# Kernel optimization log

Measured on AMD Instinct MI355X. Metric: run time of the kernel, lower is better.

## Reference

```python
import jax, jax.numpy as jnp
import numpy as np

C = 512
NH = 8
GROUPS = 32
EPS = 1e-5


def setup_inputs() -> dict:
    key = jax.random.key(0)
    ks = jax.random.split(key, 7)
    B, T, H, W = 4, 24, 32, 32
    x = jax.random.normal(ks[0], (B, C, T, H, W), dtype=jnp.float32)
    gn_w = jnp.ones((C,), jnp.float32)
    gn_b = jnp.zeros((C,), jnp.float32)
    # 1x1 Conv1d weights stored as [out_ch, in_ch] (kernel dim of size 1 dropped)
    qkv_w = jax.random.normal(ks[1], (3 * C, C), dtype=jnp.float32) / np.sqrt(C)
    qkv_b = jax.random.normal(ks[2], (3 * C,), dtype=jnp.float32) * 0.02
    proj_w = jax.random.normal(ks[3], (C, C), dtype=jnp.float32) / np.sqrt(C)
    proj_b = jax.random.normal(ks[4], (C,), dtype=jnp.float32) * 0.02
    return {"x": x, "gn_w": gn_w, "gn_b": gn_b, "qkv_w": qkv_w,
            "qkv_b": qkv_b, "proj_w": proj_w, "proj_b": proj_b}


def reference(x, gn_w, gn_b, qkv_w, qkv_b, proj_w, proj_b):
    B, Cc, T, H, W = x.shape
    hd = Cc // NH
    # [B,C,T,H,W] -> [B*H*W, C, T]
    xf = jnp.transpose(x, (0, 3, 4, 1, 2)).reshape(B * H * W, Cc, T)
    # GroupNorm over (C/G, T) per group
    xg = xf.reshape(-1, GROUPS, Cc // GROUPS, T)
    mean = xg.mean(axis=(2, 3), keepdims=True)
    var = xg.var(axis=(2, 3), keepdims=True)
    xn = ((xg - mean) * jax.lax.rsqrt(var + EPS)).reshape(-1, Cc, T)
    xn = xn * gn_w[:, None] + gn_b[:, None]
    # 1x1 conv QKV: [n, 3C, T]
    qkv = jnp.einsum('nct,dc->ndt', xn, qkv_w) + qkv_b[:, None]
    qkv = qkv.reshape(-1, 3, NH, hd, T)
    q, k, v = qkv[:, 0], qkv[:, 1], qkv[:, 2]  # each [n, h, d, T]
    scale = 1.0 / np.sqrt(hd)
    attn = jax.nn.softmax(jnp.einsum('nhdt,nhds->nhts', q, k) * scale, axis=-1)
    out = jnp.einsum('nhts,nhds->nhtd', attn, v)        # [n, h, T, d]
    out = out.transpose(0, 2, 1, 3).reshape(-1, T, Cc)   # [n, T, C]
    out = out.transpose(0, 2, 1)                         # [n, C, T]
    out = jnp.einsum('nct,dc->ndt', out, proj_w) + proj_b[:, None]
    out = out.reshape(B, H, W, Cc, T).transpose(0, 3, 4, 1, 2)
    return x + out
```

## Files before the change

### kernel.cpp

```cpp
#include <hip/hip_runtime.h>
#include <hip/hip_bf16.h>
#include <stdint.h>

#define C_    512
#define T_    24
#define HWSZ  1024
#define NN    4096
#define JTOT  98304
#define EPSV  1e-5f

typedef short short8 __attribute__((ext_vector_type(8)));
typedef short short4v __attribute__((ext_vector_type(4)));
typedef float f32x4 __attribute__((ext_vector_type(4)));
typedef float f32x2 __attribute__((ext_vector_type(2)));
typedef __bf16 bf16x2 __attribute__((ext_vector_type(2)));

typedef __attribute__((address_space(1))) const uint32_t glob_u32;
typedef __attribute__((address_space(3))) uint32_t lds_u32;

#if __has_builtin(__builtin_amdgcn_fdot2_f32_bf16)
#define HAS_DOT2 1
#else
#define HAS_DOT2 0
#endif

__device__ __forceinline__ unsigned short f2bf(float f) {
  union { float f; unsigned u; } v; v.f = f;
  unsigned r = v.u + 0x7fffu + ((v.u >> 16) & 1u);
  return (unsigned short)(r >> 16);
}
__device__ __forceinline__ float bf2f(unsigned short b) {
  union { unsigned u; float f; } v; v.u = ((unsigned)b) << 16;
  return v.f;
}
__device__ __forceinline__ float bflo(uint32_t u) {
  union { unsigned u; float f; } v; v.u = u << 16; return v.f;
}
__device__ __forceinline__ float bfhi(uint32_t u) {
  union { unsigned u; float f; } v; v.u = u & 0xffff0000u; return v.f;
}
__device__ __forceinline__ uint32_t pkbf(float a, float b) {
  return (uint32_t)f2bf(a) | ((uint32_t)f2bf(b) << 16);
}
__device__ __forceinline__ bf16x2 asbf2(uint32_t u) {
  union { uint32_t u; bf16x2 v; } c; c.u = u; return c.v;
}

__device__ __forceinline__ void gload_lds16(const void* g, void* l) {
  __builtin_amdgcn_global_load_lds((glob_u32*)g, (lds_u32*)l, 16, 0, 0);
}

__global__ void k_cvt(const float* __restrict__ qkvw, const float* __restrict__ projw,
                      unsigned short* __restrict__ qkvw_bf, unsigned short* __restrict__ projw_bf) {
  int i = blockIdx.x * 256 + threadIdx.x;
  if (i < 786432) qkvw_bf[i] = f2bf(qkvw[i]);
  if (i < 262144) projw_bf[i] = f2bf(projw[i]);
}

__global__ __launch_bounds__(256) void k_stats(const float* __restrict__ x,
                                               float* __restrict__ mean, float* __restrict__ rstd) {
  int bid = blockIdx.x;
  int g = bid & 31, hwt = (bid >> 5) & 15, b = bid >> 9;
  int tid = threadIdx.x, lane = tid & 63, grp = tid >> 6;
  int hw = hwt * 64 + lane;
  float s = 0.f, sq = 0.f;
  for (int ct = grp; ct < 384; ct += 4) {
    int c = g * 16 + ct / 24;
    int t = ct % 24;
    float v = x[((size_t)((b * 512 + c) * 24 + t) << 10) + hw];
    s += v; sq += v * v;
  }
  __shared__ float ls[4][64], lq[4][64];
  ls[grp][lane] = s; lq[grp][lane] = sq;
  __syncthreads();
  if (tid < 64) {
    float S = ls[0][tid] + ls[1][tid] + ls[2][tid] + ls[3][tid];
    float Q = lq[0][tid] + lq[1][tid] + lq[2][tid] + lq[3][tid];
    float m = S * (1.f / 384.f);
    float var = Q * (1.f / 384.f) - m * m;
    int n = b * HWSZ + hwt * 64 + tid;
    mean[n * 32 + g] = m;
    rstd[n * 32 + g] = rsqrtf(var + EPSV);
  }
}

__global__ __launch_bounds__(256) void k_norm(const float* __restrict__ x,
                                              const float* __restrict__ mean, const float* __restrict__ rstd,
                                              const float* __restrict__ gnw, const float* __restrict__ gnb,
                                              unsigned short* __restrict__ xn) {
  __shared__ unsigned short xs[64][260];
  const int bid = blockIdx.x;
  const int hwt = bid & 15;
  const int chalf = (bid >> 4) & 1;
  const int tb = bid >> 5;
  const int t = tb % 24, b = tb / 24;
  const int hw0 = hwt * 64;
  const int tid = threadIdx.x;
  const int w = tid >> 6, lane = tid & 63;

  const int cslot = w * 4 + (lane >> 4);
  const int hwr = (lane & 15) * 4;
#pragma unroll
  for (int k = 0; k < 8; ++k) {
    const int crel = k * 32 + cslot * 2;
    const int c = chalf * 256 + crel;
    const float4 v0 = *reinterpret_cast<const float4*>(
        &x[(((size_t)(b * 512 + c) * 24 + t) << 10) + hw0 + hwr]);
    const float4 v1 = *reinterpret_cast<const float4*>(
        &x[(((size_t)(b * 512 + c + 1) * 24 + t) << 10) + hw0 + hwr]);
    *reinterpret_cast<uint32_t*>(&xs[hwr + 0][crel]) = pkbf(v0.x, v1.x);
    *reinterpret_cast<uint32_t*>(&xs[hwr + 1][crel]) = pkbf(v0.y, v1.y);
    *reinterpret_cast<uint32_t*>(&xs[hwr + 2][crel]) = pkbf(v0.z, v1.z);
    *reinterpret_cast<uint32_t*>(&xs[hwr + 3][crel]) = pkbf(v0.w, v1.w);
  }

  const int crel8 = (lane & 31) * 8;
  const int c8 = chalf * 256 + crel8;
  const int g = c8 >> 4;
  float gw[8], gb[8];
#pragma unroll
  for (int i = 0; i < 8; ++i) { gw[i] = gnw[c8 + i]; gb[i] = gnb[c8 + i]; }
  float mm[8], rr[8];
#pragma unroll
  for (int p = 0; p < 8; ++p) {
    const int nrel = (p * 4 + w) * 2 + (lane >> 5);
    const int ng = b * HWSZ + hw0 + nrel;
    mm[p] = mean[ng * 32 + g];
    rr[p] = rstd[ng * 32 + g];
  }
  __syncthreads();

#pragma unroll
  for (int p = 0; p < 8; ++p) {
    const int nrel = (p * 4 + w) * 2 + (lane >> 5);
    const short4v lo = *reinterpret_cast<const short4v*>(&xs[nrel][crel8]);
    const short4v hi = *reinterpret_cast<const short4v*>(&xs[nrel][crel8 + 4]);
    float y[8];
#pragma unroll
    for (int i = 0; i < 4; ++i) {
      y[i]     = (bf2f((unsigned short)lo[i]) - mm[p]) * rr[p] * gw[i]     + gb[i];
      y[i + 4] = (bf2f((unsigned short)hi[i]) - mm[p]) * rr[p] * gw[i + 4] + gb[i + 4];
    }
    uint4 wv;
    wv.x = pkbf(y[0], y[1]);
    wv.y = pkbf(y[2], y[3]);
    wv.z = pkbf(y[4], y[5]);
    wv.w = pkbf(y[6], y[7]);
    const size_t j = (size_t)t * NN + b * HWSZ + hw0 + nrel;
    *reinterpret_cast<uint4*>(&xn[j * C_ + c8]) = wv;
  }
}

#define STAGE8(mat, half, tile, Gptr, row0)                                           \
  {                                                                                   \
    unsigned short* _l = &lds[(((tile) & 1) * 2 + (mat))][half][(w * 2) * 512];       \
    const unsigned short* _g = (Gptr) +                                               \
        (size_t)((row0) + (half) * 128 + (w * 2) * 8 + srow) * 512 +                  \
        (tile) * 64 + sslot * 8;                                                      \
    gload_lds16(_g, _l);                                                              \
    gload_lds16(_g + 8 * 512, _l + 512);                                              \
  }

__global__ __launch_bounds__(512, 2) void k_gemm8(
    const unsigned short* __restrict__ A,
    const unsigned short* __restrict__ B,
    const float* __restrict__ bias,
    uint32_t* __restrict__ outP) {
  __shared__ __attribute__((aligned(16))) unsigned short lds[4][2][8192];
  const int bid = blockIdx.x;
  const int cpx = 2304 >> 3;
  const int lid = (bid & 7) * cpx + (bid >> 3);
  const int mt = lid % 6, jt = lid / 6;
  const int m0 = mt * 256, j0 = jt * 256;
  const int tid = threadIdx.x;
  const int w = tid >> 6, lane = tid & 63;
  const int l16 = lane & 15, lqq = lane >> 4;
  const int wm = w >> 2, wn = w & 3;
  const int srow = lane >> 3;
  const int sslot = (lane & 7) ^ srow;
  const int k0off = l16 * 64 + ((lqq ^ (l16 & 7)) * 8);
  const int k1off = l16 * 64 + (((lqq + 4) ^ (l16 & 7)) * 8);

  f32x4 acc[8][4];
#pragma unroll
  for (int i = 0; i < 8; ++i)
#pragma unroll
    for (int j = 0; j < 4; ++j) acc[i][j] = {0.f, 0.f, 0.f, 0.f};

  STAGE8(0, 0, 0, A, m0); STAGE8(0, 1, 0, A, m0);
  STAGE8(1, 0, 0, B, j0); STAGE8(1, 1, 0, B, j0);
  STAGE8(0, 0, 1, A, m0); STAGE8(0, 1, 1, A, m0);
  STAGE8(1, 0, 1, B, j0);
  asm volatile("s_waitcnt vmcnt(6)" ::: "memory");
  __builtin_amdgcn_s_barrier();

  for (int t = 0; t < 8; ++t) {
    const int buf = t & 1;
    const unsigned short* Ab = &lds[buf * 2 + 0][wm][0];
    const unsigned short* Bb = &lds[buf * 2 + 1][wn >> 1][(wn & 1) * 4096];
    short8 a[8][2], bb[4][2];
#pragma unroll
    for (int rr = 0; rr < 8; ++rr) {
      a[rr][0] = *reinterpret_cast<const short8*>(Ab + rr * 1024 + k0off);
      a[rr][1] = *reinterpret_cast<const short8*>(Ab + rr * 1024 + k1off);
    }
#pragma unroll
    for (int cc = 0; cc < 2; ++cc) {
      bb[cc][0] = *reinterpret_cast<const short8*>(Bb + cc * 1024 + k0off);
      bb[cc][1] = *reinterpret_cast<const short8*>(Bb + cc * 1024 + k1off);
    }
    if (t < 7) STAGE8(1, 1, t + 1, B, j0);
    asm volatile("" ::: "memory");
    __builtin_amdgcn_s_barrier();
    asm volatile("s_waitcnt lgkmcnt(0)" ::: "memory");
    __builtin_amdgcn_sched_barrier(0);
    __builtin_amdgcn_s_setprio(1);
#pragma unroll
    for (int rr = 0; rr < 4; ++rr)
#pragma unroll
      for (int cc = 0; cc < 2; ++cc) {
        acc[rr][cc] = __builtin_amdgcn_mfma_f32_16x16x32_bf16(a[rr][0], bb[cc][0], acc[rr][cc], 0, 0, 0);
        acc[rr][cc] = __builtin_amdgcn_mfma_f32_16x16x32_bf16(a[rr][1], bb[cc][1], acc[rr][cc], 0, 0, 0);
      }
    __builtin_amdgcn_s_setprio(0);
    asm volatile("" ::: "memory");
    __builtin_amdgcn_s_barrier();
#pragma unroll
    for (int cc = 2; cc < 4; ++cc) {
      bb[cc][0] = *reinterpret_cast<const short8*>(Bb + cc * 1024 + k0off);
      bb[cc][1] = *reinterpret_cast<const short8*>(Bb + cc * 1024 + k1off);
    }
    if (t < 6) STAGE8(0, 0, t + 2, A, m0);
    asm volatile("" ::: "memory");
    __builtin_amdgcn_s_barrier();
    asm volatile("s_waitcnt lgkmcnt(0)" ::: "memory");
    __builtin_amdgcn_sched_barrier(0);
    __builtin_amdgcn_s_setprio(1);
#pragma unroll
    for (int rr = 0; rr < 4; ++rr)
#pragma unroll
      for (int cc = 2; cc < 4; ++cc) {
        acc[rr][cc] = __builtin_amdgcn_mfma_f32_16x16x32_bf16(a[rr][0], bb[cc][0], acc[rr][cc], 0, 0, 0);
        acc[rr][cc] = __builtin_amdgcn_mfma_f32_16x16x32_bf16(a[rr][1], bb[cc][1], acc[rr][cc], 0, 0, 0);
      }
    __builtin_amdgcn_s_setprio(0);
    asm volatile("" ::: "memory");
    __builtin_amdgcn_s_barrier();
    if (t < 6) STAGE8(0, 1, t + 2, A, m0);
    asm volatile("" ::: "memory");
    __builtin_amdgcn_s_barrier();
    __builtin_amdgcn_s_setprio(1);
#pragma unroll
    for (int rr = 4; rr < 8; ++rr)
#pragma unroll
      for (int cc = 0; cc < 2; ++cc) {
        acc[rr][cc] = __builtin_amdgcn_mfma_f32_16x16x32_bf16(a[rr][0], bb[cc][0], acc[rr][cc], 0, 0, 0);
        acc[rr][cc] = __builtin_amdgcn_mfma_f32_16x16x32_bf16(a[rr][1], bb[cc][1], acc[rr][cc], 0, 0, 0);
      }
    __builtin_amdgcn_s_setprio(0);
    asm volatile("" ::: "memory");
    __builtin_amdgcn_s_barrier();
    if (t < 6) STAGE8(1, 0, t + 2, B, j0);
    asm volatile("" ::: "memory");
    __builtin_amdgcn_s_barrier();
    __builtin_amdgcn_s_setprio(1);
#pragma unroll
    for (int rr = 4; rr < 8; ++rr)
#pragma unroll
      for (int cc = 2; cc < 4; ++cc) {
        acc[rr][cc] = __builtin_amdgcn_mfma_f32_16x16x32_bf16(a[rr][0], bb[cc][0], acc[rr][cc], 0, 0, 0);
        acc[rr][cc] = __builtin_amdgcn_mfma_f32_16x16x32_bf16(a[rr][1], bb[cc][1], acc[rr][cc], 0, 0, 0);
      }
    __builtin_amdgcn_s_setprio(0);
    asm volatile("" ::: "memory");
    if (t < 6) {
      asm volatile("s_waitcnt vmcnt(6)" ::: "memory");
    } else if (t == 6) {
      asm volatile("s_waitcnt vmcnt(0)" ::: "memory");
    }
    __builtin_amdgcn_s_barrier();
  }

#pragma unroll
  for (int rr = 0; rr < 8; ++rr) {
#pragma unroll
    for (int cc = 0; cc < 4; ++cc) {
      const int row = m0 + wm * 128 + rr * 16 + lqq * 4;
      const int col = j0 + wn * 64 + cc * 16 + l16;
      const int t_ = col >> 12, n = col & 4095;
      const int mat = row >> 9;
      const int hh = (row >> 6) & 7;
      const int d = row & 63;
      const int ch = d >> 3;
      const int dp = (d & 7) >> 1;
      const size_t blk = (size_t)((((mat * 8 + hh) * 8 + ch) * 4 + dp) * 24 + t_);
      const float v0 = acc[rr][cc][0] + bias[row];
      const float v1 = acc[rr][cc][1] + bias[row + 1];
      const float v2 = acc[rr][cc][2] + bias[row + 2];
      const float v3 = acc[rr][cc][3] + bias[row + 3];
      outP[blk * 4096 + n] = pkbf(v0, v1);
      outP[(blk + 24) * 4096 + n] = pkbf(v2, v3);
    }
  }
}

__global__ __launch_bounds__(256, 3) void k_proj(
    const unsigned short* __restrict__ A,
    const unsigned short* __restrict__ B,
    const float* __restrict__ bias,
    const float* __restrict__ xres,
    float* __restrict__ outf) {
  __shared__ __attribute__((aligned(16))) unsigned short As[2][8192];
  const int bid = blockIdx.x;
  const int cpx = 3072 >> 3;
  const int lid = (bid & 7) * cpx + (bid >> 3);
  const int mt = lid & 3, jt = lid >> 2;
  const int m0 = mt * 128, j0 = jt * 128;
  const int tid = threadIdx.x;
  const int w = tid >> 6, lane = tid & 63;
  const int l16 = lane & 15, lqq = lane >> 4;
  const int wm = w >> 1, wn = w & 1;
  const int srow8 = lane >> 3;
  const int sslot = (lane & 7) ^ srow8;
  const int k0off = l16 * 64 + ((lqq ^ (l16 & 7)) * 8);
  const int k1off = l16 * 64 + (((lqq + 4) ^ (l16 & 7)) * 8);

  f32x4 acc[4][4];
#pragma unroll
  for (int i = 0; i < 4; ++i)
#pragma unroll
    for (int j = 0; j < 4; ++j) acc[i][j] = {0.f, 0.f, 0.f, 0.f};

#define PSTAGE(buf, tile)                                                             \
  {                                                                                   \
    _Pragma("unroll")                                                                 \
    for (int m_ = 0; m_ < 4; ++m_) {                                                  \
      unsigned short* _l = &As[buf][m_ * 2048 + w * 512];                             \
      const unsigned short* _g = A +                                                  \
          (size_t)(m0 + m_ * 32 + w * 8 + srow8) * 512 + (tile) * 64 + sslot * 8;     \
      gload_lds16(_g, _l);                                                            \
    }                                                                                 \
  }

#define LOADB(dst, tt)                                                                \
  {                                                                                   \
    _Pragma("unroll")                                                                 \
    for (int cc = 0; cc < 4; ++cc) {                                                  \
      const int jj_ = j0 + wn * 64 + cc * 16 + l16;                                   \
      _Pragma("unroll")                                                               \
      for (int ks = 0; ks < 2; ++ks)                                                  \
        dst[cc][ks] = *reinterpret_cast<const short8*>(                               \
            &B[((size_t)((tt) * 8 + ks * 4 + lqq) * JTOT + jj_) * 8]);                \
    }                                                                                 \
  }

#define PSTEP(t, CUR, NXT)                                                            \
  {                                                                                   \
    if ((t) < 7) { PSTAGE(((t) + 1) & 1, (t) + 1); LOADB(NXT, (t) + 1); }             \
    const unsigned short* Ab = &As[(t) & 1][(wm * 64) * 64];                          \
    _Pragma("unroll")                                                                 \
    for (int rr = 0; rr < 4; ++rr) {                                                  \
      short8 a0 = *reinterpret_cast<const short8*>(Ab + rr * 1024 + k0off);           \
      short8 a1 = *reinterpret_cast<const short8*>(Ab + rr * 1024 + k1off);           \
      _Pragma("unroll")                                                               \
      for (int cc = 0; cc < 4; ++cc) {                                                \
        acc[rr][cc] = __builtin_amdgcn_mfma_f32_16x16x32_bf16(a0, CUR[cc][0], acc[rr][cc], 0, 0, 0); \
        acc[rr][cc] = __builtin_amdgcn_mfma_f32_16x16x32_bf16(a1, CUR[cc][1], acc[rr][cc], 0, 0, 0); \
      }                                                                               \
    }                                                                                 \
    __syncthreads();                                                                  \
  }

  short8 bbA[4][2], bbB[4][2];
  PSTAGE(0, 0);
  LOADB(bbA, 0);
  __syncthreads();

  PSTEP(0, bbA, bbB);
  PSTEP(1, bbB, bbA);
  PSTEP(2, bbA, bbB);
  PSTEP(3, bbB, bbA);
  PSTEP(4, bbA, bbB);
  PSTEP(5, bbB, bbA);
  PSTEP(6, bbA, bbB);
  PSTEP(7, bbB, bbA);

#pragma unroll
  for (int mi = 0; mi < 4; ++mi) {
#pragma unroll
    for (int ni = 0; ni < 4; ++ni) {
      const int dbase = m0 + wm * 64 + mi * 16 + lqq * 4;
      const int jj = j0 + wn * 64 + ni * 16 + l16;
      const int t_ = jj >> 12, n = jj & 4095;
      const int b_ = n >> 10, hw = n & 1023;
#pragma unroll
      for (int r = 0; r < 4; ++r) {
        size_t o = (((size_t)(b_ * 512 + dbase + r) * 24 + t_) << 10) + hw;
        outf[o] = xres[o] + acc[mi][ni][r] + bias[dbase + r];
      }
    }
  }
}

__global__ __launch_bounds__(512) void k_attn(const uint32_t* __restrict__ qkvP,
                                              unsigned short* __restrict__ aoC) {
  __shared__ uint32_t kq[2][4][24][64];
  const int ntile = blockIdx.x, h = blockIdx.y;
  const int n0 = ntile * 64;
  const int tid = threadIdx.x;
  const int lane = tid & 63, slot = tid >> 6;
  const int t0 = slot * 3;
  uint32_t* kqf = &kq[0][0][0][0];
  const int BLK = 4 * 24 * 4096;
  const size_t bQ = (size_t)((0 * 8 + h) * 8) * BLK;
  const size_t bK = (size_t)((1 * 8 + h) * 8) * BLK;
  const size_t bV = (size_t)((2 * 8 + h) * 8) * BLK;
  const int ub = tid & 448;

#define STAGE_QK(c_)                                                                  \
  {                                                                                   \
    const size_t cbk = bK + (size_t)(c_) * BLK;                                       \
    const size_t cbq = bQ + (size_t)(c_) * BLK;                                       \
    _Pragma("unroll")                                                                 \
    for (int p = 0; p < 3; ++p) {                                                     \
      const int u = p * 512 + tid;                                                    \
      gload_lds16(qkvP + cbk + (u >> 4) * 4096 + n0 + (u & 15) * 4,                   \
                  kqf + (size_t)(p * 512 + ub) * 4);                                  \
    }                                                                                 \
    _Pragma("unroll")                                                                 \
    for (int p = 0; p < 3; ++p) {                                                     \
      const int u = p * 512 + tid;                                                    \
      gload_lds16(qkvP + cbq + (u >> 4) * 4096 + n0 + (u & 15) * 4,                   \
                  kqf + (size_t)(1536 + p * 512 + ub) * 4);                           \
    }                                                                                 \
  }

#define STAGE_V(c_)                                                                   \
  {                                                                                   \
    const size_t cbv = bV + (size_t)(c_) * BLK;                                       \
    _Pragma("unroll")                                                                 \
    for (int p = 0; p < 3; ++p) {                                                     \
      const int u = p * 512 + tid;                                                    \
      gload_lds16(qkvP + cbv + (u >> 4) * 4096 + n0 + (u & 15) * 4,                   \
                  kqf + (size_t)(p * 512 + ub) * 4);                                  \
    }                                                                                 \
  }

  float S[3][24];
#pragma unroll
  for (int a = 0; a < 3; ++a)
#pragma unroll
    for (int s = 0; s < 24; ++s) S[a][s] = 0.f;

  STAGE_QK(0);
  __syncthreads();
  for (int c = 0; c < 8; ++c) {
    uint32_t qw[3][4];
#pragma unroll
    for (int dp = 0; dp < 4; ++dp)
#pragma unroll
      for (int a = 0; a < 3; ++a)
        qw[a][dp] = kq[1][dp][t0 + a][lane];
#if !HAS_DOT2
    float qf[3][8];
#pragma unroll
    for (int dp = 0; dp < 4; ++dp)
#pragma unroll
      for (int a = 0; a < 3; ++a) {
        qf[a][2 * dp]     = bflo(qw[a][dp]);
        qf[a][2 * dp + 1] = bfhi(qw[a][dp]);
      }
#endif
#pragma unroll
    for (int dp = 0; dp < 4; ++dp) {
#pragma unroll
      for (int s = 0; s < 24; ++s) {
        const uint32_t kpr = kq[0][dp][s][lane];
#if HAS_DOT2
        const bf16x2 k2 = asbf2(kpr);
        S[0][s] = __builtin_amdgcn_fdot2_f32_bf16(asbf2(qw[0][dp]), k2, S[0][s], false);
        S[1][s] = __builtin_amdgcn_fdot2_f32_bf16(asbf2(qw[1][dp]), k2, S[1][s], false);
        S[2][s] = __builtin_amdgcn_fdot2_f32_bf16(asbf2(qw[2][dp]), k2, S[2][s], false);
#else
        const float k0 = bflo(kpr), k1 = bfhi(kpr);
        S[0][s] = fmaf(qf[0][2 * dp], k0, S[0][s]);
        S[0][s] = fmaf(qf[0][2 * dp + 1], k1, S[0][s]);
        S[1][s] = fmaf(qf[1][2 * dp], k0, S[1][s]);
        S[1][s] = fmaf(qf[1][2 * dp + 1], k1, S[1][s]);
        S[2][s] = fmaf(qf[2][2 * dp], k0, S[2][s]);
        S[2][s] = fmaf(qf[2][2 * dp + 1], k1, S[2][s]);
#endif
      }
    }
    __syncthreads();
    if (c < 7) {
      STAGE_QK(c + 1);
      __syncthreads();
    }
  }

#pragma unroll
  for (int a = 0; a < 3; ++a) {
    float mx = S[a][0];
#pragma unroll
    for (int s = 1; s < 24; ++s) mx = fmaxf(mx, S[a][s]);
    float sum = 0.f;
#pragma unroll
    for (int s = 0; s < 24; ++s) {
      float e = __expf((S[a][s] - mx) * 0.125f);
      S[a][s] = e; sum += e;
    }
    float inv = 1.f / sum;
#pragma unroll
    for (int s = 0; s < 24; ++s) S[a][s] *= inv;
  }

  STAGE_V(0);
  __syncthreads();
  for (int c = 0; c < 8; ++c) {
    f32x2 o2[3][4];
#pragma unroll
    for (int a = 0; a < 3; ++a)
#pragma unroll
      for (int dp = 0; dp < 4; ++dp) o2[a][dp] = {0.f, 0.f};
#pragma unroll
    for (int dp = 0; dp < 4; ++dp) {
#pragma unroll
      for (int s = 0; s < 24; ++s) {
        const uint32_t vpr = kq[0][dp][s][lane];
        f32x2 v2;
        v2.x = bflo(vpr);
        v2.y = bfhi(vpr);
        o2[0][dp] += S[0][s] * v2;
        o2[1][dp] += S[1][s] * v2;
        o2[2][dp] += S[2][s] * v2;
      }
    }
#pragma unroll
    for (int a = 0; a < 3; ++a) {
      uint4 wv;
      wv.x = pkbf(o2[a][0].x, o2[a][0].y);
      wv.y = pkbf(o2[a][1].x, o2[a][1].y);
      wv.z = pkbf(o2[a][2].x, o2[a][2].y);
      wv.w = pkbf(o2[a][3].x, o2[a][3].y);
      const size_t unit = (size_t)(h * 8 + c) * JTOT + (size_t)(t0 + a) * NN + n0 + lane;
      *reinterpret_cast<uint4*>(&aoC[unit * 8]) = wv;
    }
    __syncthreads();
    if (c < 7) {
      STAGE_V(c + 1);
      __syncthreads();
    }
  }
}

extern "C" void kernel_launch(void* const* d_in, const int* in_sizes, int n_in,
                              void* d_out, int out_size, void* d_ws, size_t ws_size,
                              hipStream_t stream) {
  (void)in_sizes; (void)n_in; (void)out_size; (void)ws_size;
  const float* x     = (const float*)d_in[0];
  const float* gnw   = (const float*)d_in[1];
  const float* gnb   = (const float*)d_in[2];
  const float* qkvw  = (const float*)d_in[3];
  const float* qkvb  = (const float*)d_in[4];
  const float* projw = (const float*)d_in[5];
  const float* projb = (const float*)d_in[6];
  float* out = (float*)d_out;
  char* ws = (char*)d_ws;

  unsigned short* qkvw_bf = (unsigned short*)(ws);
  unsigned short* projw_bf = (unsigned short*)(ws + 1572864);
  float* mean = (float*)(ws + 2097152);
  float* rstd = (float*)(ws + 2621440);
  unsigned short* xn  = (unsigned short*)(ws + 3145728);
  uint32_t* qkvP = (uint32_t*)(ws + 3145728 + 100663296);

  k_cvt<<<dim3(3072), dim3(256), 0, stream>>>(qkvw, projw, qkvw_bf, projw_bf);
  k_stats<<<dim3(2048), dim3(256), 0, stream>>>(x, mean, rstd);
  k_norm<<<dim3(3072), dim3(256), 0, stream>>>(x, mean, rstd, gnw, gnb, xn);
  k_gemm8<<<dim3(2304), dim3(512), 0, stream>>>(qkvw_bf, xn, qkvb, qkvP);
  k_attn<<<dim3(64, 8), dim3(512), 0, stream>>>(qkvP, xn);
  k_proj<<<dim3(3072), dim3(256), 0, stream>>>(projw_bf, xn, projb, x, out);
}
```

Before: 533.0 us.

## Interleave QKV packed layout so each token's 8 head dims form one 16-byte unit

Changes the QKV GEMM epilogue to write the four bf16 pairs of an 8-dim chunk contiguously per (t, n), using 8-byte vector stores in place of two scattered 4-byte stores. The attention kernel now loads these 16-byte units with global-to-LDS copies and reads them from shared memory as uint4, cutting LDS read instructions fourfold and making the global stores more contiguous. The cost is a different LDS access pattern, where wide reads may hit more bank conflicts, and changed register pressure in the unrolled loops.

```diff
diff --git a/kernel.cpp b/kernel.cpp
--- a/kernel.cpp
+++ b/kernel.cpp
@@ -293,13 +293,11 @@
       const int d = row & 63;
       const int ch = d >> 3;
       const int dp = (d & 7) >> 1;
-      const size_t blk = (size_t)((((mat * 8 + hh) * 8 + ch) * 4 + dp) * 24 + t_);
-      const float v0 = acc[rr][cc][0] + bias[row];
-      const float v1 = acc[rr][cc][1] + bias[row + 1];
-      const float v2 = acc[rr][cc][2] + bias[row + 2];
-      const float v3 = acc[rr][cc][3] + bias[row + 3];
-      outP[blk * 4096 + n] = pkbf(v0, v1);
-      outP[(blk + 24) * 4096 + n] = pkbf(v2, v3);
+      const size_t base = (size_t)((mat * 8 + hh) * 8 + ch) * 393216;
+      uint2 st;
+      st.x = pkbf(acc[rr][cc][0] + bias[row], acc[rr][cc][1] + bias[row + 1]);
+      st.y = pkbf(acc[rr][cc][2] + bias[row + 2], acc[rr][cc][3] + bias[row + 3]);
+      *reinterpret_cast<uint2*>(&outP[base + ((size_t)t_ * 4096 + n) * 4 + dp]) = st;
     }
   }
 }
@@ -404,47 +402,35 @@
 
 __global__ __launch_bounds__(512) void k_attn(const uint32_t* __restrict__ qkvP,
                                               unsigned short* __restrict__ aoC) {
-  __shared__ uint32_t kq[2][4][24][64];
+  __shared__ uint4 kq[2][1536];
   const int ntile = blockIdx.x, h = blockIdx.y;
   const int n0 = ntile * 64;
   const int tid = threadIdx.x;
   const int lane = tid & 63, slot = tid >> 6;
   const int t0 = slot * 3;
-  uint32_t* kqf = &kq[0][0][0][0];
-  const int BLK = 4 * 24 * 4096;
+  const int BLK = 393216;
   const size_t bQ = (size_t)((0 * 8 + h) * 8) * BLK;
   const size_t bK = (size_t)((1 * 8 + h) * 8) * BLK;
   const size_t bV = (size_t)((2 * 8 + h) * 8) * BLK;
   const int ub = tid & 448;
 
-#define STAGE_QK(c_)                                                                  \
+#define STAGE_M(cbase, dstbuf)                                                        \
   {                                                                                   \
-    const size_t cbk = bK + (size_t)(c_) * BLK;                                       \
-    const size_t cbq = bQ + (size_t)(c_) * BLK;                                       \
     _Pragma("unroll")                                                                 \
     for (int p = 0; p < 3; ++p) {                                                     \
       const int u = p * 512 + tid;                                                    \
-      gload_lds16(qkvP + cbk + (u >> 4) * 4096 + n0 + (u & 15) * 4,                   \
-                  kqf + (size_t)(p * 512 + ub) * 4);                                  \
+      gload_lds16(qkvP + (cbase) + ((size_t)(u >> 6) * 4096 + n0 + (u & 63)) * 4,     \
+                  (void*)(&kq[dstbuf][p * 512 + ub]));                                \
     }                                                                                 \
-    _Pragma("unroll")                                                                 \
-    for (int p = 0; p < 3; ++p) {                                                     \
-      const int u = p * 512 + tid;                                                    \
-      gload_lds16(qkvP + cbq + (u >> 4) * 4096 + n0 + (u & 15) * 4,                   \
-                  kqf + (size_t)(1536 + p * 512 + ub) * 4);                           \
-    }                                                                                 \
-  }
-
-#define STAGE_V(c_)                                                                   \
+  }
+
+#define STAGE_QK(c_)                                                                  \
   {                                                                                   \
-    const size_t cbv = bV + (size_t)(c_) * BLK;                                       \
-    _Pragma("unroll")                                                                 \
-    for (int p = 0; p < 3; ++p) {                                                     \
-      const int u = p * 512 + tid;                                                    \
-      gload_lds16(qkvP + cbv + (u >> 4) * 4096 + n0 + (u & 15) * 4,                   \
-                  kqf + (size_t)(p * 512 + ub) * 4);                                  \
-    }                                                                                 \
-  }
+    STAGE_M(bK + (size_t)(c_) * BLK, 0);                                              \
+    STAGE_M(bQ + (size_t)(c_) * BLK, 1);                                              \
+  }
+
+#define STAGE_V(c_) { STAGE_M(bV + (size_t)(c_) * BLK, 0); }
 
   float S[3][24];
 #pragma unroll
@@ -455,42 +441,41 @@
   STAGE_QK(0);
   __syncthreads();
   for (int c = 0; c < 8; ++c) {
-    uint32_t qw[3][4];
-#pragma unroll
-    for (int dp = 0; dp < 4; ++dp)
-#pragma unroll
-      for (int a = 0; a < 3; ++a)
-        qw[a][dp] = kq[1][dp][t0 + a][lane];
+    uint4 qv[3];
+#pragma unroll
+    for (int a = 0; a < 3; ++a) qv[a] = kq[1][(t0 + a) * 64 + lane];
 #if !HAS_DOT2
     float qf[3][8];
 #pragma unroll
-    for (int dp = 0; dp < 4; ++dp)
+    for (int a = 0; a < 3; ++a) {
+      qf[a][0] = bflo(qv[a].x); qf[a][1] = bfhi(qv[a].x);
+      qf[a][2] = bflo(qv[a].y); qf[a][3] = bfhi(qv[a].y);
+      qf[a][4] = bflo(qv[a].z); qf[a][5] = bfhi(qv[a].z);
+      qf[a][6] = bflo(qv[a].w); qf[a][7] = bfhi(qv[a].w);
+    }
+#endif
+#pragma unroll
+    for (int s = 0; s < 24; ++s) {
+      const uint4 kk = kq[0][s * 64 + lane];
+#if HAS_DOT2
 #pragma unroll
       for (int a = 0; a < 3; ++a) {
-        qf[a][2 * dp]     = bflo(qw[a][dp]);
-        qf[a][2 * dp + 1] = bfhi(qw[a][dp]);
+        S[a][s] = __builtin_amdgcn_fdot2_f32_bf16(asbf2(qv[a].x), asbf2(kk.x), S[a][s], false);
+        S[a][s] = __builtin_amdgcn_fdot2_f32_bf16(asbf2(qv[a].y), asbf2(kk.y), S[a][s], false);
+        S[a][s] = __builtin_amdgcn_fdot2_f32_bf16(asbf2(qv[a].z), asbf2(kk.z), S[a][s], false);
+        S[a][s] = __builtin_amdgcn_fdot2_f32_bf16(asbf2(qv[a].w), asbf2(kk.w), S[a][s], false);
+      }
+#else
+      const float k0 = bflo(kk.x), k1 = bfhi(kk.x), k2 = bflo(kk.y), k3 = bfhi(kk.y);
+      const float k4 = bflo(kk.z), k5 = bfhi(kk.z), k6 = bflo(kk.w), k7 = bfhi(kk.w);
+#pragma unroll
+      for (int a = 0; a < 3; ++a) {
+        S[a][s] = fmaf(qf[a][0], k0, S[a][s]); S[a][s] = fmaf(qf[a][1], k1, S[a][s]);
+        S[a][s] = fmaf(qf[a][2], k2, S[a][s]); S[a][s] = fmaf(qf[a][3], k3, S[a][s]);
+        S[a][s] = fmaf(qf[a][4], k4, S[a][s]); S[a][s] = fmaf(qf[a][5], k5, S[a][s]);
+        S[a][s] = fmaf(qf[a][6], k6, S[a][s]); S[a][s] = fmaf(qf[a][7], k7, S[a][s]);
       }
 #endif
-#pragma unroll
-    for (int dp = 0; dp < 4; ++dp) {
-#pragma unroll
-      for (int s = 0; s < 24; ++s) {
-        const uint32_t kpr = kq[0][dp][s][lane];
-#if HAS_DOT2
-        const bf16x2 k2 = asbf2(kpr);
-        S[0][s] = __builtin_amdgcn_fdot2_f32_bf16(asbf2(qw[0][dp]), k2, S[0][s], false);
-        S[1][s] = __builtin_amdgcn_fdot2_f32_bf16(asbf2(qw[1][dp]), k2, S[1][s], false);
-        S[2][s] = __builtin_amdgcn_fdot2_f32_bf16(asbf2(qw[2][dp]), k2, S[2][s], false);
-#else
-        const float k0 = bflo(kpr), k1 = bfhi(kpr);
-        S[0][s] = fmaf(qf[0][2 * dp], k0, S[0][s]);
-        S[0][s] = fmaf(qf[0][2 * dp + 1], k1, S[0][s]);
-        S[1][s] = fmaf(qf[1][2 * dp], k0, S[1][s]);
-        S[1][s] = fmaf(qf[1][2 * dp + 1], k1, S[1][s]);
-        S[2][s] = fmaf(qf[2][2 * dp], k0, S[2][s]);
-        S[2][s] = fmaf(qf[2][2 * dp + 1], k1, S[2][s]);
-#endif
-      }
     }
     __syncthreads();
     if (c < 7) {
@@ -524,16 +509,19 @@
 #pragma unroll
       for (int dp = 0; dp < 4; ++dp) o2[a][dp] = {0.f, 0.f};
 #pragma unroll
-    for (int dp = 0; dp < 4; ++dp) {
-#pragma unroll
-      for (int s = 0; s < 24; ++s) {
-        const uint32_t vpr = kq[0][dp][s][lane];
-        f32x2 v2;
-        v2.x = bflo(vpr);
-        v2.y = bfhi(vpr);
-        o2[0][dp] += S[0][s] * v2;
-        o2[1][dp] += S[1][s] * v2;
-        o2[2][dp] += S[2][s] * v2;
+    for (int s = 0; s < 24; ++s) {
+      const uint4 vv = kq[0][s * 64 + lane];
+      f32x2 v0, v1, v2, v3;
+      v0.x = bflo(vv.x); v0.y = bfhi(vv.x);
+      v1.x = bflo(vv.y); v1.y = bfhi(vv.y);
+      v2.x = bflo(vv.z); v2.y = bfhi(vv.z);
+      v3.x = bflo(vv.w); v3.y = bfhi(vv.w);
+#pragma unroll
+      for (int a = 0; a < 3; ++a) {
+        o2[a][0] += S[a][s] * v0;
+        o2[a][1] += S[a][s] * v1;
+        o2[a][2] += S[a][s] * v2;
+        o2[a][3] += S[a][s] * v3;
       }
     }
 #pragma unroll
```

Result: faster. 513.2 us, median of 2 (-3.7%).
